# Kernel optimization log

Measured on AMD Instinct MI355X. Metric: run time of the kernel, lower is better.

## Reference

```python
import jax, jax.numpy as jnp
import numpy as np

NUM_CLASSES = 100000
FEAT_DIM = 512
BATCH = 16384
ALPHA = 0.5
LAMDA = 0.003


def setup_inputs() -> dict:
    key = jax.random.key(0)
    k1, k2, k3, k4 = jax.random.split(key, 4)
    inputs = jax.random.normal(k1, (BATCH, FEAT_DIM), dtype=jnp.float32)
    centers = jax.random.normal(k2, (NUM_CLASSES, FEAT_DIM), dtype=jnp.float32)  # init_scheme='normal'
    weight_per_class = jax.random.uniform(k3, (NUM_CLASSES,), dtype=jnp.float32)
    targets = jax.random.randint(k4, (BATCH,), 0, NUM_CLASSES, dtype=jnp.int32)
    return {"inputs": inputs, "centers": centers, "weight_per_class": weight_per_class, "targets": targets}


def reference(inputs, centers, weight_per_class, targets):
    # --- gather + elementwise weighted half-MSE (reduction='none') ---
    target_centers = centers[targets]                      # [B, D] gather
    diff = inputs - target_centers
    loss = (diff * diff) * 0.5                             # [B, D]

    # per-sample class weights, broadcast to [B, D], scaled by lamda
    tw = LAMDA * weight_per_class[targets]                 # [B]
    target_weights = jnp.broadcast_to(tw[:, None], loss.shape)

    # --- center update: per-class sum(inputs) / (1 + count), done as scatter-add
    # (equivalent to the original dense one-hot [C, B, D] expansion) ---
    num = jax.ops.segment_sum(inputs, targets, num_segments=NUM_CLASSES)      # [C, D]
    counts = jax.ops.segment_sum(jnp.ones((inputs.shape[0],), dtype=inputs.dtype),
                                 targets, num_segments=NUM_CLASSES)           # [C]
    center_deltas = num / (1.0 + counts)[:, None]
    new_centers = centers - ALPHA * center_deltas          # in-place buffer update in torch

    return (loss, target_weights, new_centers)
```

## Files before the change

### kernel.cpp

```cpp
#include <hip/hip_runtime.h>

#define BATCH 16384
#define FEAT  512
#define NCLS  100000
#define KCAP  16
#define ALPHA 0.5f
#define LAMDA 0.003f

__global__ void wcl_bucket_kernel(const int* __restrict__ targets,
                                  int* __restrict__ counts,
                                  int* __restrict__ buckets) {
    int b = blockIdx.x * blockDim.x + threadIdx.x;
    if (b < BATCH) {
        int t = targets[b];
        int slot = atomicAdd(&counts[t], 1);
        if (slot < KCAP) buckets[(size_t)t * KCAP + slot] = b;
    }
}

__global__ void __launch_bounds__(128)
wcl_class_kernel(const float* __restrict__ inputs,
                 const float* __restrict__ centers,
                 const float* __restrict__ wpc,
                 const int* __restrict__ counts,
                 const int* __restrict__ buckets,
                 float* __restrict__ loss,
                 float* __restrict__ tw,
                 float* __restrict__ out_centers) {
    int c = blockIdx.x;
    int d = threadIdx.x;

    const float4 cv = ((const float4*)(centers + (size_t)c * FEAT))[d];
    float4* orow = (float4*)(out_centers + (size_t)c * FEAT);

    int cnt = counts[c];
    if (cnt == 0) {
        orow[d] = cv;
        return;
    }

    float w = LAMDA * wpc[c];
    float4 wv = make_float4(w, w, w, w);
    float4 acc = make_float4(0.f, 0.f, 0.f, 0.f);

    int n = cnt < KCAP ? cnt : KCAP;
    for (int s = 0; s < n; ++s) {
        int b = buckets[(size_t)c * KCAP + s];
        float4 x = ((const float4*)(inputs + (size_t)b * FEAT))[d];
        acc.x += x.x; acc.y += x.y; acc.z += x.z; acc.w += x.w;

        float4 l;
        float dx = x.x - cv.x; l.x = 0.5f * dx * dx;
        float dy = x.y - cv.y; l.y = 0.5f * dy * dy;
        float dz = x.z - cv.z; l.z = 0.5f * dz * dz;
        float dw = x.w - cv.w; l.w = 0.5f * dw * dw;

        ((float4*)(loss + (size_t)b * FEAT))[d] = l;
        ((float4*)(tw   + (size_t)b * FEAT))[d] = wv;
    }

    float coef = ALPHA / (1.0f + (float)cnt);
    float4 o;
    o.x = cv.x - coef * acc.x;
    o.y = cv.y - coef * acc.y;
    o.z = cv.z - coef * acc.z;
    o.w = cv.w - coef * acc.w;
    orow[d] = o;
}

extern "C" void kernel_launch(void* const* d_in, const int* in_sizes, int n_in,
                              void* d_out, int out_size, void* d_ws, size_t ws_size,
                              hipStream_t stream) {
    const float* inputs  = (const float*)d_in[0];
    const float* centers = (const float*)d_in[1];
    const float* wpc     = (const float*)d_in[2];
    const int*   targets = (const int*)d_in[3];

    float* loss        = (float*)d_out;
    float* tw          = loss + (size_t)BATCH * FEAT;
    float* out_centers = tw   + (size_t)BATCH * FEAT;

    int* counts  = (int*)d_ws;
    int* buckets = counts + NCLS;
    hipMemsetAsync(counts, 0, (size_t)NCLS * sizeof(int), stream);

    wcl_bucket_kernel<<<(BATCH + 255) / 256, 256, 0, stream>>>(targets, counts, buckets);

    wcl_class_kernel<<<NCLS, 128, 0, stream>>>(
        inputs, centers, wpc, counts, buckets, loss, tw, out_centers);
}
```

Measured before the change: 432.5 us.

## Split center update into bulk copy kernel and compacted dirty-class kernel

The bucket kernel now also builds a compacted list of classes that received at least one sample. A grid-stride copy kernel writes the untouched center rows, and a persistent kernel with a fixed grid walks only the dirty classes to compute loss, weights and updated centers. This replaces the 100k-block launch, where most blocks only copied a row, with dense streaming copies and a small grid for the scattered work. It adds an extra kernel launch and a per-element count lookup in the copy kernel.

```diff
diff --git a/kernel.cpp b/kernel.cpp
--- a/kernel.cpp
+++ b/kernel.cpp
@@ -7,65 +7,83 @@
 #define ALPHA 0.5f
 #define LAMDA 0.003f
 
+
 __global__ void wcl_bucket_kernel(const int* __restrict__ targets,
                                   int* __restrict__ counts,
+                                  int* __restrict__ ndirty,
+                                  int* __restrict__ dirty,
                                   int* __restrict__ buckets) {
     int b = blockIdx.x * blockDim.x + threadIdx.x;
     if (b < BATCH) {
         int t = targets[b];
         int slot = atomicAdd(&counts[t], 1);
         if (slot < KCAP) buckets[(size_t)t * KCAP + slot] = b;
+        if (slot == 0) {
+            int i = atomicAdd(ndirty, 1);
+            dirty[i] = t;
+        }
+    }
+}
+
+__global__ void __launch_bounds__(256)
+wcl_copy_kernel(const float4* __restrict__ src,
+                float4* __restrict__ dst,
+                const int* __restrict__ counts) {
+    const size_t n = (size_t)NCLS * (FEAT / 4);
+    const size_t stride = (size_t)gridDim.x * blockDim.x;
+    for (size_t i = (size_t)blockIdx.x * blockDim.x + threadIdx.x; i < n; i += stride) {
+        int c = (int)(i >> 7);
+        if (counts[c] == 0) {
+            dst[i] = src[i];
+        }
     }
 }
 
 __global__ void __launch_bounds__(128)
-wcl_class_kernel(const float* __restrict__ inputs,
+wcl_dirty_kernel(const float* __restrict__ inputs,
                  const float* __restrict__ centers,
                  const float* __restrict__ wpc,
                  const int* __restrict__ counts,
+                 const int* __restrict__ ndirty,
+                 const int* __restrict__ dirty,
                  const int* __restrict__ buckets,
                  float* __restrict__ loss,
                  float* __restrict__ tw,
                  float* __restrict__ out_centers) {
-    int c = blockIdx.x;
     int d = threadIdx.x;
+    int nd = *ndirty;
+    for (int i = blockIdx.x; i < nd; i += gridDim.x) {
+        int c = dirty[i];
+        const float4 cv = ((const float4*)(centers + (size_t)c * FEAT))[d];
+        int cnt = counts[c];
+        float w = LAMDA * wpc[c];
+        float4 wv = make_float4(w, w, w, w);
+        float4 acc = make_float4(0.f, 0.f, 0.f, 0.f);
 
-    const float4 cv = ((const float4*)(centers + (size_t)c * FEAT))[d];
-    float4* orow = (float4*)(out_centers + (size_t)c * FEAT);
+        int m = cnt < KCAP ? cnt : KCAP;
+        for (int s = 0; s < m; ++s) {
+            int b = buckets[(size_t)c * KCAP + s];
+            float4 x = ((const float4*)(inputs + (size_t)b * FEAT))[d];
+            acc.x += x.x; acc.y += x.y; acc.z += x.z; acc.w += x.w;
 
-    int cnt = counts[c];
-    if (cnt == 0) {
-        orow[d] = cv;
-        return;
+            float4 l;
+            float dx = x.x - cv.x; l.x = 0.5f * dx * dx;
+            float dy = x.y - cv.y; l.y = 0.5f * dy * dy;
+            float dz = x.z - cv.z; l.z = 0.5f * dz * dz;
+            float dw = x.w - cv.w; l.w = 0.5f * dw * dw;
+
+            ((float4*)(loss + (size_t)b * FEAT))[d] = l;
+            ((float4*)(tw   + (size_t)b * FEAT))[d] = wv;
+        }
+
+        float coef = ALPHA / (1.0f + (float)cnt);
+        float4 o;
+        o.x = cv.x - coef * acc.x;
+        o.y = cv.y - coef * acc.y;
+        o.z = cv.z - coef * acc.z;
+        o.w = cv.w - coef * acc.w;
+        ((float4*)(out_centers + (size_t)c * FEAT))[d] = o;
     }
-
-    float w = LAMDA * wpc[c];
-    float4 wv = make_float4(w, w, w, w);
-    float4 acc = make_float4(0.f, 0.f, 0.f, 0.f);
-
-    int n = cnt < KCAP ? cnt : KCAP;
-    for (int s = 0; s < n; ++s) {
-        int b = buckets[(size_t)c * KCAP + s];
-        float4 x = ((const float4*)(inputs + (size_t)b * FEAT))[d];
-        acc.x += x.x; acc.y += x.y; acc.z += x.z; acc.w += x.w;
-
-        float4 l;
-        float dx = x.x - cv.x; l.x = 0.5f * dx * dx;
-        float dy = x.y - cv.y; l.y = 0.5f * dy * dy;
-        float dz = x.z - cv.z; l.z = 0.5f * dz * dz;
-        float dw = x.w - cv.w; l.w = 0.5f * dw * dw;
-
-        ((float4*)(loss + (size_t)b * FEAT))[d] = l;
-        ((float4*)(tw   + (size_t)b * FEAT))[d] = wv;
-    }
-
-    float coef = ALPHA / (1.0f + (float)cnt);
-    float4 o;
-    o.x = cv.x - coef * acc.x;
-    o.y = cv.y - coef * acc.y;
-    o.z = cv.z - coef * acc.z;
-    o.w = cv.w - coef * acc.w;
-    orow[d] = o;
 }
 
 extern "C" void kernel_launch(void* const* d_in, const int* in_sizes, int n_in,
@@ -81,11 +99,19 @@
     float* out_centers = tw   + (size_t)BATCH * FEAT;
 
     int* counts  = (int*)d_ws;
-    int* buckets = counts + NCLS;
-    hipMemsetAsync(counts, 0, (size_t)NCLS * sizeof(int), stream);
+    int* ndirty  = counts + NCLS;
+    int* dirty   = ndirty + 1;
+    int* buckets = dirty + NCLS;
 
-    wcl_bucket_kernel<<<(BATCH + 255) / 256, 256, 0, stream>>>(targets, counts, buckets);
+    hipMemsetAsync(counts, 0, (size_t)(NCLS + 1) * sizeof(int), stream);
 
-    wcl_class_kernel<<<NCLS, 128, 0, stream>>>(
-        inputs, centers, wpc, counts, buckets, loss, tw, out_centers);
+    wcl_bucket_kernel<<<(BATCH + 255) / 256, 256, 0, stream>>>(
+        targets, counts, ndirty, dirty, buckets);
+
+    wcl_copy_kernel<<<2048, 256, 0, stream>>>(
+        (const float4*)centers, (float4*)out_centers, counts);
+
+    wcl_dirty_kernel<<<4096, 128, 0, stream>>>(
+        inputs, centers, wpc, counts, ndirty, dirty, buckets,
+        loss, tw, out_centers);
 }
```

Measured after the change: 451.8 us. +4.5%, slower.
